# Kernel optimization log

Measured on AMD Instinct MI355X. Metric: run time of the kernel, lower is better.

Reference implementation:

```python
import jax, jax.numpy as jnp
import numpy as np

P = 32
EPS = 1e-5

def setup_inputs() -> dict:
    key = jax.random.key(0)
    ks = jax.random.split(key, 6)
    B, C, H, W = 2, 256, 512, 512
    h_past = jax.random.normal(ks[0], (B, C, H, W), dtype=jnp.float32)
    scale = jnp.ones((C,), jnp.float32)
    shift = jnp.zeros((C,), jnp.float32)
    # depthwise 3x3: torch Conv2d(ch, ch, 3, groups=ch) weight shape (C,1,3,3)
    dw_w = jax.random.normal(ks[1], (C, 1, 3, 3), dtype=jnp.float32) * (1.0 / 3.0)
    dw_b = jax.random.normal(ks[2], (C,), dtype=jnp.float32) * 0.02
    # pointwise 1x1: weight (C_out, C_in)
    pw_w = jax.random.normal(ks[3], (C, C), dtype=jnp.float32) * (1.0 / np.sqrt(C))
    pw_b = jax.random.normal(ks[4], (C,), dtype=jnp.float32) * 0.02
    return {"h_past": h_past, "scale": scale, "shift": shift,
            "dw_w": dw_w, "dw_b": dw_b, "pw_w": pw_w, "pw_b": pw_b}

def reference(h_past, scale, shift, dw_w, dw_b, pw_w, pw_b):
    B, C, H, W = h_past.shape
    NRp, NCp = H // P, W // P
    # block-mean pool: [B,C,NRp,P,NCp,P] -> [B,C,NRp,NCp]
    x = h_past.reshape(B, C, NRp, P, NCp, P).mean(axis=(3, 5))
    # channel norm (mean/var over channel dim, unbiased=False)
    mu = x.mean(axis=1, keepdims=True)
    var = x.var(axis=1, keepdims=True)
    x = (x - mu) * jax.lax.rsqrt(var + EPS)
    x = x * scale[None, :, None, None] + shift[None, :, None, None]
    # depthwise 3x3 conv, padding=1
    x = jax.lax.conv_general_dilated(
        x, dw_w, window_strides=(1, 1), padding=((1, 1), (1, 1)),
        feature_group_count=C,
        dimension_numbers=("NCHW", "OIHW", "NCHW"))
    x = x + dw_b[None, :, None, None]
    # exact GELU (torch F.gelu default)
    x = jax.nn.gelu(x, approximate=False)
    # pointwise 1x1 conv
    x = jnp.einsum("bchw,oc->bohw", x, pw_w) + pw_b[None, :, None, None]
    # broadcast-upsample back to full H x W
    x_full = jnp.broadcast_to(x[:, :, :, None, :, None], (B, C, NRp, P, NCp, P))
    return x_full.reshape(B, C, NRp * P, NCp * P)
```

## Files before the change

kernel.cpp:

```cpp
#include <hip/hip_runtime.h>
#include <math.h>

constexpr int B = 2, C = 256, H = 512, W = 512, P = 32;
constexpr int NR = H / P;
constexpr int NC = W / P;
constexpr int NPOS = NR * NC;
constexpr float EPS = 1e-5f;

typedef float floatx4 __attribute__((ext_vector_type(4)));

__global__ void pool_kernel(const float* __restrict__ h_past,
                            float* __restrict__ xp) {
    int bid = blockIdx.x;
    int br = bid & 15;
    int c  = (bid >> 4) & 255;
    int b  = bid >> 12;
    const floatx4* src =
        (const floatx4*)(h_past + (((size_t)(b * C + c)) * H + (size_t)br * P) * W);
    int t    = threadIdx.x;
    int f4   = t & 127;
    int row0 = t >> 7;
    float s = 0.f;
#pragma unroll
    for (int k = 0; k < 16; ++k) {
        floatx4 v = __builtin_nontemporal_load(&src[(row0 + 2 * k) * 128 + f4]);
        s += v.x + v.y + v.z + v.w;
    }
    __shared__ float part[256];
    part[t] = s;
    __syncthreads();
    if (t < 16) {
        float acc = 0.f;
#pragma unroll
        for (int j = 0; j < 8; ++j)
            acc += part[t * 8 + j] + part[128 + t * 8 + j];
        xp[((size_t)(b * NPOS + br * NC + t)) * C + c] = acc * (1.0f / (P * P));
    }
}

__global__ void stats_kernel(const float* __restrict__ xp,
                             float* __restrict__ mu_arr,
                             float* __restrict__ rs_arr) {
    int bid = blockIdx.x;
    int t = threadIdx.x;
    float v = xp[(size_t)bid * C + t];
    __shared__ float red[8];
    float s = v;
#pragma unroll
    for (int off = 32; off > 0; off >>= 1) s += __shfl_down(s, off, 64);
    int wave = t >> 6, lane = t & 63;
    if (lane == 0) red[wave] = s;
    __syncthreads();
    float mu = (red[0] + red[1] + red[2] + red[3]) * (1.0f / C);
    float d = v - mu;
    float s2 = d * d;
#pragma unroll
    for (int off = 32; off > 0; off >>= 1) s2 += __shfl_down(s2, off, 64);
    if (lane == 0) red[4 + wave] = s2;
    __syncthreads();
    if (t == 0) {
        float var = (red[4] + red[5] + red[6] + red[7]) * (1.0f / C);
        mu_arr[bid] = mu;
        rs_arr[bid] = rsqrtf(var + EPS);
    }
}

__device__ inline float gelu_exact(float x) {
    return 0.5f * x * (1.0f + erff(x * 0.70710678118654752440f));
}

__global__ void fused_kernel(const float* __restrict__ xp,
                             const float* __restrict__ mu_arr,
                             const float* __restrict__ rs_arr,
                             const float* __restrict__ scale,
                             const float* __restrict__ shift,
                             const float* __restrict__ dw_w,
                             const float* __restrict__ dw_b,
                             const float* __restrict__ pw_w,
                             const float* __restrict__ pw_b,
                             float* __restrict__ z) {
    int bid = blockIdx.x;
    int p = bid & 255;
    int b = bid >> 8;
    int h = p >> 4;
    int w = p & 15;
    int c = threadIdx.x;

    float sc = scale[c];
    float sh = shift[c];
    const float* wt  = dw_w + c * 9;
    const float* xpb = xp + (size_t)b * NPOS * C;
    const float* mub = mu_arr + b * NPOS;
    const float* rsb = rs_arr + b * NPOS;

    float acc = 0.f;
#pragma unroll
    for (int kh = 0; kh < 3; ++kh) {
        int hh = h + kh - 1;
        if (hh < 0 || hh >= NR) continue;
#pragma unroll
        for (int kw = 0; kw < 3; ++kw) {
            int ww = w + kw - 1;
            if (ww < 0 || ww >= NC) continue;
            int q = hh * NC + ww;
            float xv = xpb[(size_t)q * C + c];
            float xn = (xv - mub[q]) * rsb[q] * sc + sh;
            acc += xn * wt[kh * 3 + kw];
        }
    }
    float yv = gelu_exact(acc + dw_b[c]);

    __shared__ float ys[256];
    ys[c] = yv;
    __syncthreads();

    const float4* wr = (const float4*)(pw_w + c * C);
    const float4* yv4 = (const float4*)ys;
    float acc2 = 0.f;
#pragma unroll 4
    for (int c4 = 0; c4 < 64; ++c4) {
        float4 wv = wr[c4];
        float4 vv = yv4[c4];
        acc2 += wv.x * vv.x + wv.y * vv.y + wv.z * vv.z + wv.w * vv.w;
    }
    z[((size_t)(b * C + c)) * NPOS + p] = acc2 + pw_b[c];
}

__global__ void up_kernel(const float* __restrict__ z,
                          floatx4* __restrict__ out) {
    const int total = B * C * H * (W / 4);
    for (int idx = blockIdx.x * 256 + threadIdx.x; idx < total;
         idx += gridDim.x * 256) {
        int w4 = idx & 127;
        int h  = (idx >> 7) & 511;
        int bc = idx >> 16;
        float v = z[bc * NPOS + (h >> 5) * NC + (w4 >> 3)];
        floatx4 o = {v, v, v, v};
        __builtin_nontemporal_store(o, &out[idx]);
    }
}

extern "C" void kernel_launch(void* const* d_in, const int* in_sizes, int n_in,
                              void* d_out, int out_size, void* d_ws, size_t ws_size,
                              hipStream_t stream) {
    const float* h_past = (const float*)d_in[0];
    const float* scale  = (const float*)d_in[1];
    const float* shift  = (const float*)d_in[2];
    const float* dw_w   = (const float*)d_in[3];
    const float* dw_b   = (const float*)d_in[4];
    const float* pw_w   = (const float*)d_in[5];
    const float* pw_b   = (const float*)d_in[6];
    float* out = (float*)d_out;

    float* ws = (float*)d_ws;
    const int SMALL = B * C * NPOS;
    float* xp = ws;
    float* z  = ws + SMALL;
    float* mu = ws + 2 * SMALL;
    float* rs = mu + B * NPOS;

    pool_kernel<<<B * C * NR, 256, 0, stream>>>(h_past, xp);
    stats_kernel<<<B * NPOS, 256, 0, stream>>>(xp, mu, rs);
    fused_kernel<<<B * NPOS, 256, 0, stream>>>(xp, mu, rs, scale, shift,
                                               dw_w, dw_b, pw_w, pw_b, z);
    up_kernel<<<32768, 256, 0, stream>>>(z, (floatx4*)out);
}
```

Measured before the change: 853.1 us.

## Transpose pointwise weights for coalesced reads and drop nontemporal hints

Adds a small kernel that rearranges the pointwise weight matrix so threads in the fused kernel read consecutive float4s instead of strided rows. The intermediate z buffer becomes position-major, and the upsample kernel indexes it accordingly. Nontemporal load/store hints are removed from the pool and upsample kernels. This adds an extra launch and less contiguous z reads in the upsample pass, and changes cache behaviour for the large streaming traffic.

```diff
diff --git a/kernel.cpp b/kernel.cpp
--- a/kernel.cpp
+++ b/kernel.cpp
@@ -23,7 +23,7 @@
     float s = 0.f;
 #pragma unroll
     for (int k = 0; k < 16; ++k) {
-        floatx4 v = __builtin_nontemporal_load(&src[(row0 + 2 * k) * 128 + f4]);
+        floatx4 v = src[(row0 + 2 * k) * 128 + f4];
         s += v.x + v.y + v.z + v.w;
     }
     __shared__ float part[256];
@@ -65,6 +65,16 @@
     }
 }
 
+__global__ void pwt_kernel(const float* __restrict__ pw_w,
+                           floatx4* __restrict__ pw_t) {
+    int idx = blockIdx.x * 256 + threadIdx.x;
+    int c4 = idx >> 8;
+    int o  = idx & 255;
+    const float* src = pw_w + o * C + 4 * c4;
+    floatx4 v = {src[0], src[1], src[2], src[3]};
+    pw_t[idx] = v;
+}
+
 __device__ inline float gelu_exact(float x) {
     return 0.5f * x * (1.0f + erff(x * 0.70710678118654752440f));
 }
@@ -76,7 +86,7 @@
                              const float* __restrict__ shift,
                              const float* __restrict__ dw_w,
                              const float* __restrict__ dw_b,
-                             const float* __restrict__ pw_w,
+                             const floatx4* __restrict__ pw_t,
                              const float* __restrict__ pw_b,
                              float* __restrict__ z) {
     int bid = blockIdx.x;
@@ -114,16 +124,15 @@
     ys[c] = yv;
     __syncthreads();
 
-    const float4* wr = (const float4*)(pw_w + c * C);
-    const float4* yv4 = (const float4*)ys;
+    const floatx4* yv4 = (const floatx4*)ys;
     float acc2 = 0.f;
 #pragma unroll 4
     for (int c4 = 0; c4 < 64; ++c4) {
-        float4 wv = wr[c4];
-        float4 vv = yv4[c4];
+        floatx4 wv = pw_t[c4 * 256 + c];
+        floatx4 vv = yv4[c4];
         acc2 += wv.x * vv.x + wv.y * vv.y + wv.z * vv.z + wv.w * vv.w;
     }
-    z[((size_t)(b * C + c)) * NPOS + p] = acc2 + pw_b[c];
+    z[(size_t)bid * C + c] = acc2 + pw_b[c];
 }
 
 __global__ void up_kernel(const float* __restrict__ z,
@@ -134,9 +143,12 @@
         int w4 = idx & 127;
         int h  = (idx >> 7) & 511;
         int bc = idx >> 16;
-        float v = z[bc * NPOS + (h >> 5) * NC + (w4 >> 3)];
+        int b  = bc >> 8;
+        int c  = bc & 255;
+        int p  = (h >> 5) * NC + (w4 >> 3);
+        float v = z[((size_t)(b * NPOS + p)) * C + c];
         floatx4 o = {v, v, v, v};
-        __builtin_nontemporal_store(o, &out[idx]);
+        out[idx] = o;
     }
 }
 
@@ -154,14 +166,16 @@
 
     float* ws = (float*)d_ws;
     const int SMALL = B * C * NPOS;
-    float* xp = ws;
-    float* z  = ws + SMALL;
-    float* mu = ws + 2 * SMALL;
-    float* rs = mu + B * NPOS;
+    float* xp   = ws;
+    float* z    = ws + SMALL;
+    float* mu   = ws + 2 * SMALL;
+    float* rs   = mu + B * NPOS;
+    floatx4* pw_t = (floatx4*)(rs + B * NPOS);
 
+    pwt_kernel<<<64, 256, 0, stream>>>(pw_w, pw_t);
     pool_kernel<<<B * C * NR, 256, 0, stream>>>(h_past, xp);
     stats_kernel<<<B * NPOS, 256, 0, stream>>>(xp, mu, rs);
     fused_kernel<<<B * NPOS, 256, 0, stream>>>(xp, mu, rs, scale, shift,
-                                               dw_w, dw_b, pw_w, pw_b, z);
+                                               dw_w, dw_b, pw_t, pw_b, z);
     up_kernel<<<32768, 256, 0, stream>>>(z, (floatx4*)out);
 }
```

New measurement: 895.7 us. 5.0% more time.
